# Optimization experiments

Hardware: AMD Instinct MI355X
Metric: run time of the kernel (lower is better)

## Reference

```python
import jax, jax.numpy as jnp
import numpy as np

N_NODES = 100000


def setup_inputs() -> dict:
    key = jax.random.key(0)
    k1, k2, k3, k4, k5 = jax.random.split(key, 5)
    n_edges = 3200000
    in_f, out_f = 256, 256
    X = jax.random.normal(k1, (N_NODES, in_f), dtype=jnp.float32)
    edge_src = jax.random.randint(k2, (n_edges,), 0, N_NODES, dtype=jnp.int32)
    edge_dst = jax.random.randint(k3, (n_edges,), 0, N_NODES, dtype=jnp.int32)
    edge_val = jax.random.uniform(k4, (n_edges,), dtype=jnp.float32)
    # kaiming-uniform-like init for weight (out_f, in_f)
    bound = np.sqrt(6.0 / in_f)
    W = jax.random.uniform(k5, (out_f, in_f), dtype=jnp.float32, minval=-bound, maxval=bound)
    b = jnp.zeros((out_f,), dtype=jnp.float32)
    return {"X": X, "edge_src": edge_src, "edge_dst": edge_dst,
            "edge_val": edge_val, "W": W, "b": b}


def reference(X, edge_src, edge_dst, edge_val, W, b):
    # S = A @ X, where A is COO sparse: A[src, dst] = val
    # gather neighbor features, scale by edge value, scatter-add to src rows
    msgs = edge_val[:, None] * X[edge_dst]              # [E, in_f]
    S = jax.ops.segment_sum(msgs, edge_src, num_segments=N_NODES)  # [N, in_f]
    # dense projection + bias: (A X) W^T + b
    return S @ W.T + b
```

## Files before the change

kernel.cpp:

```cpp
#include <hip/hip_runtime.h>

#define NNODES 100000
#define F 256
#define NBKT ((NNODES + 127) / 128)
#define BKT_CAP 5120
#define CHUNK_A 8192

typedef unsigned short u16;
typedef unsigned int   u32;
typedef __attribute__((ext_vector_type(8))) short short8v;
typedef __attribute__((ext_vector_type(8))) unsigned short ushort8;
typedef __attribute__((ext_vector_type(4))) float f32x4;
typedef __attribute__((ext_vector_type(2))) float f32x2;

__device__ __forceinline__ u16 f2bf(float f) {
    u32 u = __float_as_uint(f);
    u32 r = u + 0x7FFFu + ((u >> 16) & 1u);
    return (u16)(r >> 16);
}

__global__ __launch_bounds__(256) void cast_w(const float* __restrict__ W,
                                              u16* __restrict__ Wb) {
    int i = blockIdx.x * 256 + threadIdx.x;
    if (i >= F * F / 4) return;
    float4 w = ((const float4*)W)[i];
    ushort4 o;
    o.x = f2bf(w.x); o.y = f2bf(w.y); o.z = f2bf(w.z); o.w = f2bf(w.w);
    ((ushort4*)Wb)[i] = o;
}

__global__ __launch_bounds__(256) void cast_x(const float* __restrict__ X,
                                              u16* __restrict__ Xb, int total4) {
    int i = blockIdx.x * 256 + threadIdx.x;
    if (i >= total4) return;
    float4 x = ((const float4*)X)[i];
    ushort4 o;
    o.x = f2bf(x.x); o.y = f2bf(x.y); o.z = f2bf(x.z); o.w = f2bf(x.w);
    ((ushort4*)Xb)[i] = o;
}

__global__ __launch_bounds__(256) void gemm_mfma(const u16* __restrict__ Xb,
                                                 const u16* __restrict__ Wb,
                                                 u16* __restrict__ Yb) {
    const int wave = threadIdx.x >> 6;
    const int lane = threadIdx.x & 63;
    const int lm   = lane & 15;
    const int kg   = lane >> 4;
    const int m0   = blockIdx.x * 128 + wave * 32;
    const int n0   = blockIdx.y * 128;

    f32x4 acc[2][8];
#pragma unroll
    for (int t = 0; t < 2; ++t)
#pragma unroll
        for (int u = 0; u < 8; ++u) acc[t][u] = (f32x4){0.f, 0.f, 0.f, 0.f};

    int rowA[2];
#pragma unroll
    for (int t = 0; t < 2; ++t) {
        int row = m0 + t * 16 + lm;
        rowA[t] = (row < NNODES) ? row : NNODES - 1;
    }

    for (int k0 = 0; k0 < F; k0 += 32) {
        const int kb = k0 + kg * 8;
        short8v aF[2];
#pragma unroll
        for (int t = 0; t < 2; ++t)
            aF[t] = *(const short8v*)(Xb + (size_t)rowA[t] * F + kb);
        short8v bF[8];
#pragma unroll
        for (int u = 0; u < 8; ++u)
            bF[u] = *(const short8v*)(Wb + (size_t)(n0 + u * 16 + lm) * F + kb);
#pragma unroll
        for (int t = 0; t < 2; ++t)
#pragma unroll
            for (int u = 0; u < 8; ++u)
                acc[t][u] = __builtin_amdgcn_mfma_f32_16x16x32_bf16(aF[t], bF[u], acc[t][u], 0, 0, 0);
    }

#pragma unroll
    for (int t = 0; t < 2; ++t) {
        int rbase = m0 + t * 16 + kg * 4;
#pragma unroll
        for (int i = 0; i < 4; ++i) {
            int row = rbase + i;
            if (row < NNODES) {
#pragma unroll
                for (int u = 0; u < 8; ++u)
                    Yb[(size_t)row * F + n0 + u * 16 + lm] = f2bf(acc[t][u][i]);
            }
        }
    }
}

__global__ __launch_bounds__(256) void init_cur(int* __restrict__ cur) {
    int i = blockIdx.x * 256 + threadIdx.x;
    if (i < NBKT) cur[i] = i * BKT_CAP;
}

__global__ __launch_bounds__(256) void bin_edges(const int* __restrict__ src,
                                                 const int* __restrict__ dst,
                                                 const float* __restrict__ val,
                                                 int* __restrict__ cur,
                                                 int2* __restrict__ temp,
                                                 int n_edges) {
    __shared__ int hist[NBKT];
    __shared__ int bas[NBKT];
    const int e0 = blockIdx.x * CHUNK_A;
    for (int i = threadIdx.x; i < NBKT; i += 256) hist[i] = 0;
    __syncthreads();

    u32 lpk[32];
#pragma unroll
    for (int k = 0; k < 32; ++k) {
        int e = e0 + k * 256 + threadIdx.x;
        if (e < n_edges) {
            int s = src[e];
            int bkt = s >> 7;
            int l = atomicAdd(&hist[bkt], 1);
            lpk[k] = (u32)l | ((u32)(s & 127) << 13) | ((u32)bkt << 20);
        }
    }
    __syncthreads();
    for (int i = threadIdx.x; i < NBKT; i += 256) {
        int c = hist[i];
        bas[i] = c ? atomicAdd(&cur[i], c) : 0;
    }
    __syncthreads();
#pragma unroll
    for (int k = 0; k < 32; ++k) {
        int e = e0 + k * 256 + threadIdx.x;
        if (e < n_edges) {
            u32 p   = lpk[k];
            int bkt = (int)(p >> 20);
            int pos = bas[bkt] + (int)(p & 0x1FFFu);
            int sl  = (int)((p >> 13) & 127u);
            temp[pos] = make_int2((sl << 20) | dst[e], __float_as_int(val[e]));
        }
    }
}

__global__ __launch_bounds__(256) void sort_bucket(const int* __restrict__ cur,
                                                   const int2* __restrict__ temp,
                                                   int2* __restrict__ pack,
                                                   int2* __restrict__ nodeseg) {
    __shared__ int2 tl[BKT_CAP];
    __shared__ int h[128];
    __shared__ int curl[128];
    const int b = blockIdx.x;
    const int base = b * BKT_CAP;
    int cnt = cur[b] - base;
    if (cnt > BKT_CAP) cnt = BKT_CAP;
    const int tid = threadIdx.x;

    if (tid < 128) h[tid] = 0;
    __syncthreads();
    for (int j = tid; j < cnt; j += 256) {
        int2 t = temp[base + j];
        tl[j] = t;
        atomicAdd(&h[t.x >> 20], 1);
    }
    __syncthreads();
    for (int off = 1; off < 128; off <<= 1) {
        int x = 0;
        if (tid < 128 && tid >= off) x = h[tid - off];
        __syncthreads();
        if (tid < 128) h[tid] += x;
        __syncthreads();
    }
    if (tid < 128) {
        int incl = h[tid];
        int prev = tid ? h[tid - 1] : 0;
        curl[tid] = base + prev;
        int node = b * 128 + tid;
        if (node < NNODES) nodeseg[node] = make_int2(base + prev, base + incl);
    }
    __syncthreads();
    for (int j = tid; j < cnt; j += 256) {
        int2 p = tl[j];
        int loc = p.x >> 20;
        int pos = atomicAdd(&curl[loc], 1);
        pack[pos] = make_int2((p.x & 0xFFFFF) << 9, p.y);
    }
}

__global__ __launch_bounds__(256) void gather_nodes(const int2* __restrict__ nodeseg,
                                                    const int2* __restrict__ pack,
                                                    const u16* __restrict__ Yb,
                                                    const float* __restrict__ bias,
                                                    float* __restrict__ out) {
    int node = blockIdx.x * 4 + (threadIdx.x >> 6);
    if (node >= NNODES) return;
    const int lane = threadIdx.x & 63;
    const int half = lane >> 5;
    const int l5   = lane & 31;
    const u32 loff = (u32)l5 * 16u;
    const char* Ybc = (const char*)Yb;

    int2 seg = nodeseg[node];
    const int beg = seg.x, end = seg.y;

    f32x2 acc2[4];
#pragma unroll
    for (int i = 0; i < 4; ++i) acc2[i] = (f32x2){0.f, 0.f};

    long long pr[8];
#pragma unroll
    for (int q = 0; q < 8; ++q) {
        int idx  = beg + 2 * q + half;
        int safe = idx < end ? idx : beg;
        pr[q] = __builtin_nontemporal_load((const long long*)&pack[safe]);
    }

    for (int j = beg; j < end; j += 16) {
        u32 off[8];
        float v[8];
#pragma unroll
        for (int q = 0; q < 8; ++q) {
            int idx = j + 2 * q + half;
            off[q] = (u32)((unsigned long long)pr[q] & 0xFFFFFFFFull);
            v[q]   = (idx < end) ? __int_as_float((int)(pr[q] >> 32)) : 0.f;
        }
        ushort8 y[8];
#pragma unroll
        for (int q = 0; q < 8; ++q)
            y[q] = *(const ushort8*)(Ybc + (off[q] + loff));
        int jn = j + 16;
#pragma unroll
        for (int q = 0; q < 8; ++q) {
            int idx  = jn + 2 * q + half;
            int safe = idx < end ? idx : end - 1;
            pr[q] = __builtin_nontemporal_load((const long long*)&pack[safe]);
        }
        __builtin_amdgcn_sched_barrier(0);
#pragma unroll
        for (int q = 0; q < 8; ++q) {
            f32x2 vv; vv[0] = v[q]; vv[1] = v[q];
            const u32* yp = (const u32*)&y[q];
#pragma unroll
            for (int i = 0; i < 4; ++i) {
                u32 pb = yp[i];
                f32x2 yy;
                yy[0] = __uint_as_float(pb << 16);
                yy[1] = __uint_as_float(pb & 0xFFFF0000u);
                acc2[i] = __builtin_elementwise_fma(yy, vv, acc2[i]);
            }
        }
    }

    float acc[8];
#pragma unroll
    for (int i = 0; i < 4; ++i) { acc[2 * i] = acc2[i][0]; acc[2 * i + 1] = acc2[i][1]; }
#pragma unroll
    for (int i = 0; i < 8; ++i) acc[i] += __shfl_xor(acc[i], 32);

    const int col = l5 * 8 + half * 4;
    float4 bv = *(const float4*)&bias[col];
    f32x4 o;
    o[0] = acc[half * 4 + 0] + bv.x;
    o[1] = acc[half * 4 + 1] + bv.y;
    o[2] = acc[half * 4 + 2] + bv.z;
    o[3] = acc[half * 4 + 3] + bv.w;
    __builtin_nontemporal_store(o, (f32x4*)&out[(size_t)node * F + col]);
}

extern "C" void kernel_launch(void* const* d_in, const int* in_sizes, int n_in,
                              void* d_out, int out_size, void* d_ws, size_t ws_size,
                              hipStream_t stream) {
    const float* X        = (const float*)d_in[0];
    const int*   edge_src = (const int*)d_in[1];
    const int*   edge_dst = (const int*)d_in[2];
    const float* edge_val = (const float*)d_in[3];
    const float* W        = (const float*)d_in[4];
    const float* b        = (const float*)d_in[5];
    float*       out      = (float*)d_out;
    const int n_edges     = in_sizes[1];

    char* base = (char*)d_ws;
    const size_t ybBytes   = (size_t)NNODES * F * sizeof(u16);
    const size_t packBytes = (size_t)NBKT * BKT_CAP * sizeof(int2);
    u16*  Yb      = (u16*)base;
    int2* pack    = (int2*)(base + ybBytes);
    int2* temp    = (int2*)(base + ybBytes + packBytes);
    u16*  Xb      = (u16*)pack;
    u16*  Wb      = (u16*)(base + ybBytes + 2 * packBytes);
    int2* nodeseg = (int2*)((char*)Wb + (size_t)F * F * sizeof(u16));
    int*  cur     = (int*)(nodeseg + NNODES);

    cast_w<<<(F * F / 4 + 255) / 256, 256, 0, stream>>>(W, Wb);
    int xt4 = NNODES * F / 4;
    cast_x<<<(xt4 + 255) / 256, 256, 0, stream>>>(X, Xb, xt4);

    dim3 ggrid((NNODES + 127) / 128, F / 128);
    gemm_mfma<<<ggrid, 256, 0, stream>>>(Xb, Wb, Yb);

    init_cur<<<(NBKT + 255) / 256, 256, 0, stream>>>(cur);
    bin_edges<<<(n_edges + CHUNK_A - 1) / CHUNK_A, 256, 0, stream>>>(edge_src, edge_dst, edge_val,
                                                                     cur, temp, n_edges);
    sort_bucket<<<NBKT, 256, 0, stream>>>(cur, temp, pack, nodeseg);

    gather_nodes<<<(NNODES + 3) / 4, 256, 0, stream>>>(nodeseg, pack, Yb, b, out);
}
```

Baseline: 599.8 us.

## Fuse X cast into GEMM, merge init kernels, enlarge binning chunks, drop gather prefetch

```diff
diff --git a/kernel.cpp b/kernel.cpp
--- a/kernel.cpp
+++ b/kernel.cpp
@@ -4,7 +4,7 @@
 #define F 256
 #define NBKT ((NNODES + 127) / 128)
 #define BKT_CAP 5120
-#define CHUNK_A 8192
+#define CHUNK_A 24576
 
 typedef unsigned short u16;
 typedef unsigned int   u32;
@@ -19,27 +19,22 @@
     return (u16)(r >> 16);
 }
 
-__global__ __launch_bounds__(256) void cast_w(const float* __restrict__ W,
-                                              u16* __restrict__ Wb) {
+__global__ __launch_bounds__(256) void cast_w_init(const float* __restrict__ W,
+                                                   u16* __restrict__ Wb,
+                                                   int* __restrict__ cur) {
     int i = blockIdx.x * 256 + threadIdx.x;
-    if (i >= F * F / 4) return;
-    float4 w = ((const float4*)W)[i];
-    ushort4 o;
-    o.x = f2bf(w.x); o.y = f2bf(w.y); o.z = f2bf(w.z); o.w = f2bf(w.w);
-    ((ushort4*)Wb)[i] = o;
-}
-
-__global__ __launch_bounds__(256) void cast_x(const float* __restrict__ X,
-                                              u16* __restrict__ Xb, int total4) {
-    int i = blockIdx.x * 256 + threadIdx.x;
-    if (i >= total4) return;
-    float4 x = ((const float4*)X)[i];
-    ushort4 o;
-    o.x = f2bf(x.x); o.y = f2bf(x.y); o.z = f2bf(x.z); o.w = f2bf(x.w);
-    ((ushort4*)Xb)[i] = o;
-}
-
-__global__ __launch_bounds__(256) void gemm_mfma(const u16* __restrict__ Xb,
+    if (i < F * F / 4) {
+        float4 w = ((const float4*)W)[i];
+        ushort4 o;
+        o.x = f2bf(w.x); o.y = f2bf(w.y); o.z = f2bf(w.z); o.w = f2bf(w.w);
+        ((ushort4*)Wb)[i] = o;
+    }
+    if (blockIdx.x == 0) {
+        for (int j = threadIdx.x; j < NBKT; j += 256) cur[j] = j * BKT_CAP;
+    }
+}
+
+__global__ __launch_bounds__(256) void gemm_mfma(const float* __restrict__ X,
                                                  const u16* __restrict__ Wb,
                                                  u16* __restrict__ Yb) {
     const int wave = threadIdx.x >> 6;
@@ -66,8 +61,17 @@
         const int kb = k0 + kg * 8;
         short8v aF[2];
 #pragma unroll
-        for (int t = 0; t < 2; ++t)
-            aF[t] = *(const short8v*)(Xb + (size_t)rowA[t] * F + kb);
+        for (int t = 0; t < 2; ++t) {
+            const float* xr = X + (size_t)rowA[t] * F + kb;
+            float4 x0 = *(const float4*)xr;
+            float4 x1 = *(const float4*)(xr + 4);
+            short8v a;
+            a[0] = (short)f2bf(x0.x); a[1] = (short)f2bf(x0.y);
+            a[2] = (short)f2bf(x0.z); a[3] = (short)f2bf(x0.w);
+            a[4] = (short)f2bf(x1.x); a[5] = (short)f2bf(x1.y);
+            a[6] = (short)f2bf(x1.z); a[7] = (short)f2bf(x1.w);
+            aF[t] = a;
+        }
         short8v bF[8];
 #pragma unroll
         for (int u = 0; u < 8; ++u)
@@ -92,11 +96,6 @@
             }
         }
     }
-}
-
-__global__ __launch_bounds__(256) void init_cur(int* __restrict__ cur) {
-    int i = blockIdx.x * 256 + threadIdx.x;
-    if (i < NBKT) cur[i] = i * BKT_CAP;
 }
 
 __global__ __launch_bounds__(256) void bin_edges(const int* __restrict__ src,
@@ -105,21 +104,21 @@
                                                  int* __restrict__ cur,
                                                  int2* __restrict__ temp,
                                                  int n_edges) {
+    __shared__ u32 lpk[CHUNK_A];
     __shared__ int hist[NBKT];
     __shared__ int bas[NBKT];
     const int e0 = blockIdx.x * CHUNK_A;
     for (int i = threadIdx.x; i < NBKT; i += 256) hist[i] = 0;
     __syncthreads();
 
-    u32 lpk[32];
-#pragma unroll
-    for (int k = 0; k < 32; ++k) {
-        int e = e0 + k * 256 + threadIdx.x;
+    for (int k = 0; k < CHUNK_A / 256; ++k) {
+        int j = k * 256 + threadIdx.x;
+        int e = e0 + j;
         if (e < n_edges) {
             int s = src[e];
             int bkt = s >> 7;
             int l = atomicAdd(&hist[bkt], 1);
-            lpk[k] = (u32)l | ((u32)(s & 127) << 13) | ((u32)bkt << 20);
+            lpk[j] = (u32)l | ((u32)(s & 127) << 15) | ((u32)bkt << 22);
         }
     }
     __syncthreads();
@@ -128,14 +127,14 @@
         bas[i] = c ? atomicAdd(&cur[i], c) : 0;
     }
     __syncthreads();
-#pragma unroll
-    for (int k = 0; k < 32; ++k) {
-        int e = e0 + k * 256 + threadIdx.x;
+    for (int k = 0; k < CHUNK_A / 256; ++k) {
+        int j = k * 256 + threadIdx.x;
+        int e = e0 + j;
         if (e < n_edges) {
-            u32 p   = lpk[k];
-            int bkt = (int)(p >> 20);
-            int pos = bas[bkt] + (int)(p & 0x1FFFu);
-            int sl  = (int)((p >> 13) & 127u);
+            u32 p   = lpk[j];
+            int bkt = (int)(p >> 22);
+            int pos = bas[bkt] + (int)(p & 0x7FFFu);
+            int sl  = (int)((p >> 15) & 127u);
             temp[pos] = make_int2((sl << 20) | dst[e], __float_as_int(val[e]));
         }
     }
@@ -205,35 +204,21 @@
 #pragma unroll
     for (int i = 0; i < 4; ++i) acc2[i] = (f32x2){0.f, 0.f};
 
-    long long pr[8];
-#pragma unroll
-    for (int q = 0; q < 8; ++q) {
-        int idx  = beg + 2 * q + half;
-        int safe = idx < end ? idx : beg;
-        pr[q] = __builtin_nontemporal_load((const long long*)&pack[safe]);
-    }
-
     for (int j = beg; j < end; j += 16) {
         u32 off[8];
         float v[8];
+        ushort8 y[8];
 #pragma unroll
         for (int q = 0; q < 8; ++q) {
             int idx = j + 2 * q + half;
-            off[q] = (u32)((unsigned long long)pr[q] & 0xFFFFFFFFull);
-            v[q]   = (idx < end) ? __int_as_float((int)(pr[q] >> 32)) : 0.f;
-        }
-        ushort8 y[8];
+            int safe = idx < end ? idx : end - 1;
+            long long raw = __builtin_nontemporal_load((const long long*)&pack[safe]);
+            off[q] = (u32)((unsigned long long)raw & 0xFFFFFFFFull);
+            v[q] = (idx < end) ? __int_as_float((int)(raw >> 32)) : 0.f;
+        }
 #pragma unroll
         for (int q = 0; q < 8; ++q)
             y[q] = *(const ushort8*)(Ybc + (off[q] + loff));
-        int jn = j + 16;
-#pragma unroll
-        for (int q = 0; q < 8; ++q) {
-            int idx  = jn + 2 * q + half;
-            int safe = idx < end ? idx : end - 1;
-            pr[q] = __builtin_nontemporal_load((const long long*)&pack[safe]);
-        }
-        __builtin_amdgcn_sched_barrier(0);
 #pragma unroll
         for (int q = 0; q < 8; ++q) {
             f32x2 vv; vv[0] = v[q]; vv[1] = v[q];
@@ -283,19 +268,15 @@
     u16*  Yb      = (u16*)base;
     int2* pack    = (int2*)(base + ybBytes);
     int2* temp    = (int2*)(base + ybBytes + packBytes);
-    u16*  Xb      = (u16*)pack;
     u16*  Wb      = (u16*)(base + ybBytes + 2 * packBytes);
     int2* nodeseg = (int2*)((char*)Wb + (size_t)F * F * sizeof(u16));
     int*  cur     = (int*)(nodeseg + NNODES);
 
-    cast_w<<<(F * F / 4 + 255) / 256, 256, 0, stream>>>(W, Wb);
-    int xt4 = NNODES * F / 4;
-    cast_x<<<(xt4 + 255) / 256, 256, 0, stream>>>(X, Xb, xt4);
+    cast_w_init<<<(F * F / 4 + 255) / 256, 256, 0, stream>>>(W, Wb, cur);
 
     dim3 ggrid((NNODES + 127) / 128, F / 128);
-    gemm_mfma<<<ggrid, 256, 0, stream>>>(Xb, Wb, Yb);
-
-    init_cur<<<(NBKT + 255) / 256, 256, 0, stream>>>(cur);
+    gemm_mfma<<<ggrid, 256, 0, stream>>>(X, Wb, Yb);
+
     bin_edges<<<(n_edges + CHUNK_A - 1) / CHUNK_A, 256, 0, stream>>>(edge_src, edge_dst, edge_val,
                                                                      cur, temp, n_edges);
     sort_bucket<<<NBKT, 256, 0, stream>>>(cur, temp, pack, nodeseg);
```

Result: no change. 609.9 us (+1.7%).

## Stage GEMM tiles in swizzled LDS, fuse init into cast_w, drop gather prefetch

Applied to the files above, without the earlier changes.

```diff
diff --git a/kernel.cpp b/kernel.cpp
--- a/kernel.cpp
+++ b/kernel.cpp
@@ -19,14 +19,17 @@
     return (u16)(r >> 16);
 }
 
-__global__ __launch_bounds__(256) void cast_w(const float* __restrict__ W,
-                                              u16* __restrict__ Wb) {
+__global__ __launch_bounds__(256) void cast_w_init(const float* __restrict__ W,
+                                                   u16* __restrict__ Wb,
+                                                   int* __restrict__ cur) {
     int i = blockIdx.x * 256 + threadIdx.x;
-    if (i >= F * F / 4) return;
-    float4 w = ((const float4*)W)[i];
-    ushort4 o;
-    o.x = f2bf(w.x); o.y = f2bf(w.y); o.z = f2bf(w.z); o.w = f2bf(w.w);
-    ((ushort4*)Wb)[i] = o;
+    if (i < F * F / 4) {
+        float4 w = ((const float4*)W)[i];
+        ushort4 o;
+        o.x = f2bf(w.x); o.y = f2bf(w.y); o.z = f2bf(w.z); o.w = f2bf(w.w);
+        ((ushort4*)Wb)[i] = o;
+    }
+    if (i < NBKT) cur[i] = i * BKT_CAP;
 }
 
 __global__ __launch_bounds__(256) void cast_x(const float* __restrict__ X,
@@ -42,11 +45,13 @@
 __global__ __launch_bounds__(256) void gemm_mfma(const u16* __restrict__ Xb,
                                                  const u16* __restrict__ Wb,
                                                  u16* __restrict__ Yb) {
-    const int wave = threadIdx.x >> 6;
+    __shared__ u16 As[128 * 128];
+    __shared__ u16 Bs[128 * 128];
+    const int wv   = threadIdx.x >> 6;
     const int lane = threadIdx.x & 63;
     const int lm   = lane & 15;
     const int kg   = lane >> 4;
-    const int m0   = blockIdx.x * 128 + wave * 32;
+    const int m0   = blockIdx.x * 128;
     const int n0   = blockIdx.y * 128;
 
     f32x4 acc[2][8];
@@ -55,33 +60,46 @@
 #pragma unroll
         for (int u = 0; u < 8; ++u) acc[t][u] = (f32x4){0.f, 0.f, 0.f, 0.f};
 
-    int rowA[2];
+#pragma unroll
+    for (int kt = 0; kt < 2; ++kt) {
+        if (kt) __syncthreads();
+#pragma unroll
+        for (int i = 0; i < 8; ++i) {
+            int q   = i * 256 + threadIdx.x;
+            int row = q >> 4;
+            int cs  = (q & 15) ^ (row & 7);
+            size_t goff = (size_t)row * 512 + kt * 256 + cs * 16;
+            *(ushort8*)&As[q * 8] = *(const ushort8*)((const char*)Xb + (size_t)m0 * 512 + goff);
+            *(ushort8*)&Bs[q * 8] = *(const ushort8*)((const char*)Wb + (size_t)n0 * 512 + goff);
+        }
+        __syncthreads();
+#pragma unroll
+        for (int s = 0; s < 4; ++s) {
+            short8v aF[2];
+#pragma unroll
+            for (int t = 0; t < 2; ++t) {
+                int r = wv * 32 + t * 16 + lm;
+                int c = (s * 4 + kg) ^ (r & 7);
+                aF[t] = *(const short8v*)&As[r * 128 + c * 8];
+            }
+            short8v bF[8];
+#pragma unroll
+            for (int u = 0; u < 8; ++u) {
+                int r = u * 16 + lm;
+                int c = (s * 4 + kg) ^ (r & 7);
+                bF[u] = *(const short8v*)&Bs[r * 128 + c * 8];
+            }
+#pragma unroll
+            for (int t = 0; t < 2; ++t)
+#pragma unroll
+                for (int u = 0; u < 8; ++u)
+                    acc[t][u] = __builtin_amdgcn_mfma_f32_16x16x32_bf16(aF[t], bF[u], acc[t][u], 0, 0, 0);
+        }
+    }
+
 #pragma unroll
     for (int t = 0; t < 2; ++t) {
-        int row = m0 + t * 16 + lm;
-        rowA[t] = (row < NNODES) ? row : NNODES - 1;
-    }
-
-    for (int k0 = 0; k0 < F; k0 += 32) {
-        const int kb = k0 + kg * 8;
-        short8v aF[2];
-#pragma unroll
-        for (int t = 0; t < 2; ++t)
-            aF[t] = *(const short8v*)(Xb + (size_t)rowA[t] * F + kb);
-        short8v bF[8];
-#pragma unroll
-        for (int u = 0; u < 8; ++u)
-            bF[u] = *(const short8v*)(Wb + (size_t)(n0 + u * 16 + lm) * F + kb);
-#pragma unroll
-        for (int t = 0; t < 2; ++t)
-#pragma unroll
-            for (int u = 0; u < 8; ++u)
-                acc[t][u] = __builtin_amdgcn_mfma_f32_16x16x32_bf16(aF[t], bF[u], acc[t][u], 0, 0, 0);
-    }
-
-#pragma unroll
-    for (int t = 0; t < 2; ++t) {
-        int rbase = m0 + t * 16 + kg * 4;
+        int rbase = m0 + wv * 32 + t * 16 + kg * 4;
 #pragma unroll
         for (int i = 0; i < 4; ++i) {
             int row = rbase + i;
@@ -92,11 +110,6 @@
             }
         }
     }
-}
-
-__global__ __launch_bounds__(256) void init_cur(int* __restrict__ cur) {
-    int i = blockIdx.x * 256 + threadIdx.x;
-    if (i < NBKT) cur[i] = i * BKT_CAP;
 }
 
 __global__ __launch_bounds__(256) void bin_edges(const int* __restrict__ src,
@@ -205,35 +218,21 @@
 #pragma unroll
     for (int i = 0; i < 4; ++i) acc2[i] = (f32x2){0.f, 0.f};
 
-    long long pr[8];
-#pragma unroll
-    for (int q = 0; q < 8; ++q) {
-        int idx  = beg + 2 * q + half;
-        int safe = idx < end ? idx : beg;
-        pr[q] = __builtin_nontemporal_load((const long long*)&pack[safe]);
-    }
-
     for (int j = beg; j < end; j += 16) {
         u32 off[8];
         float v[8];
+        ushort8 y[8];
 #pragma unroll
         for (int q = 0; q < 8; ++q) {
             int idx = j + 2 * q + half;
-            off[q] = (u32)((unsigned long long)pr[q] & 0xFFFFFFFFull);
-            v[q]   = (idx < end) ? __int_as_float((int)(pr[q] >> 32)) : 0.f;
-        }
-        ushort8 y[8];
+            int safe = idx < end ? idx : end - 1;
+            long long raw = __builtin_nontemporal_load((const long long*)&pack[safe]);
+            off[q] = (u32)((unsigned long long)raw & 0xFFFFFFFFull);
+            v[q] = (idx < end) ? __int_as_float((int)(raw >> 32)) : 0.f;
+        }
 #pragma unroll
         for (int q = 0; q < 8; ++q)
             y[q] = *(const ushort8*)(Ybc + (off[q] + loff));
-        int jn = j + 16;
-#pragma unroll
-        for (int q = 0; q < 8; ++q) {
-            int idx  = jn + 2 * q + half;
-            int safe = idx < end ? idx : end - 1;
-            pr[q] = __builtin_nontemporal_load((const long long*)&pack[safe]);
-        }
-        __builtin_amdgcn_sched_barrier(0);
 #pragma unroll
         for (int q = 0; q < 8; ++q) {
             f32x2 vv; vv[0] = v[q]; vv[1] = v[q];
@@ -288,14 +287,13 @@
     int2* nodeseg = (int2*)((char*)Wb + (size_t)F * F * sizeof(u16));
     int*  cur     = (int*)(nodeseg + NNODES);
 
-    cast_w<<<(F * F / 4 + 255) / 256, 256, 0, stream>>>(W, Wb);
+    cast_w_init<<<(F * F / 4 + 255) / 256, 256, 0, stream>>>(W, Wb, cur);
     int xt4 = NNODES * F / 4;
     cast_x<<<(xt4 + 255) / 256, 256, 0, stream>>>(X, Xb, xt4);
 
     dim3 ggrid((NNODES + 127) / 128, F / 128);
     gemm_mfma<<<ggrid, 256, 0, stream>>>(Xb, Wb, Yb);
 
-    init_cur<<<(NBKT + 255) / 256, 256, 0, stream>>>(cur);
     bin_edges<<<(n_edges + CHUNK_A - 1) / CHUNK_A, 256, 0, stream>>>(edge_src, edge_dst, edge_val,
                                                                      cur, temp, n_edges);
     sort_bucket<<<NBKT, 256, 0, stream>>>(cur, temp, pack, nodeseg);
```

Result: faster. 552.6 us (-7.9%).
